# Performance work log

Measured on AMD Instinct MI355X. Metric: run time of the kernel, lower is better.

The kernel has to match this reference:

```python
import jax, jax.numpy as jnp
import numpy as np

BINS = 32


def _mi_from_hist(hist):
    # hist: (B, BINS, BINS) raw counts. Normalize and compute MI per sample,
    # matching np.histogram2d marginals (px from axis=1 sum, py from axis=0 sum).
    total = jnp.sum(hist, axis=(1, 2), keepdims=True)
    p = hist / total                      # joint pmf (B, BINS, BINS)
    px = jnp.sum(p, axis=2)               # (B, BINS)
    py = jnp.sum(p, axis=1)               # (B, BINS)
    denom = px[:, :, None] * py[:, None, :]
    pos = p > 0                           # p>0 implies px>0 and py>0
    ratio = jnp.where(pos, p / jnp.where(pos, denom, 1.0), 1.0)
    mi = jnp.sum(jnp.where(pos, p * jnp.log(ratio), 0.0), axis=(1, 2))
    return mi                             # (B,)


def setup_inputs() -> dict:
    key = jax.random.key(0)
    k1, k2 = jax.random.split(key)
    shape = (32, 2, 512, 512)
    return {
        "input": jax.random.normal(k1, shape, dtype=jnp.float32),
        "target": jax.random.normal(k2, shape, dtype=jnp.float32),
    }


def reference(input, target):
    B = input.shape[0]
    u = (input.reshape(B, -1) + 1.0) / 2.0   # (B, N) mapped to ~[0,1]
    v = (target.reshape(B, -1) + 1.0) / 2.0
    # np.histogram2d with range [[0,1],[0,1]] drops out-of-range points and
    # includes the right edge in the last bin.
    in_range = (u >= 0) & (u <= 1) & (v >= 0) & (v <= 1)
    w = in_range.astype(u.dtype)
    iu = jnp.clip(jnp.floor(u * BINS).astype(jnp.int32), 0, BINS - 1)
    iv = jnp.clip(jnp.floor(v * BINS).astype(jnp.int32), 0, BINS - 1)
    flat = (jnp.arange(B, dtype=jnp.int32)[:, None] * (BINS * BINS)
            + iu * BINS + iv).reshape(-1)
    hist = jax.ops.segment_sum(w.reshape(-1), flat,
                               num_segments=B * BINS * BINS)
    hist = hist.reshape(B, BINS, BINS)
    mi = _mi_from_hist(hist)
    return -jnp.mean(mi)
```

## Files before the change

### kernel.cpp

```cpp
#include <hip/hip_runtime.h>


#define BINS 32
#define NBINS2 1024
#define LDS_ROW 33
#define LDS_HIST (BINS * LDS_ROW)
#define NBATCH 32
#define N_PER_BATCH (2 * 512 * 512)
#define NVEC_BATCH (N_PER_BATCH / 4)
#define BPB 64
#define THREADS 256
#define VPT 8

__global__ __launch_bounds__(THREADS) void hist_kernel(const float* __restrict__ x,
                                                       const float* __restrict__ y,
                                                       unsigned* __restrict__ parts) {
    __shared__ unsigned h[LDS_HIST];
    for (int i = threadIdx.x; i < LDS_HIST; i += THREADS) h[i] = 0u;
    __syncthreads();

    const int b   = blockIdx.x >> 6;
    const int blk = blockIdx.x & 63;
    const float4* xb = (const float4*)x + (size_t)b * NVEC_BATCH;
    const float4* yb = (const float4*)y + (size_t)b * NVEC_BATCH;

    const int off = blk * THREADS + threadIdx.x;
    float4 xa[VPT], ya[VPT];
#pragma unroll
    for (int j = 0; j < VPT; ++j) xa[j] = xb[(size_t)j * (BPB * THREADS) + off];
#pragma unroll
    for (int j = 0; j < VPT; ++j) ya[j] = yb[(size_t)j * (BPB * THREADS) + off];

#pragma unroll
    for (int j = 0; j < VPT; ++j) {
        float ax[4] = {xa[j].x, xa[j].y, xa[j].z, xa[j].w};
        float ty[4] = {ya[j].x, ya[j].y, ya[j].z, ya[j].w};
#pragma unroll
        for (int k = 0; k < 4; ++k) {
            float u = (ax[k] + 1.0f) * 0.5f;
            float v = (ty[k] + 1.0f) * 0.5f;
            bool ok = (u >= 0.0f) & (u <= 1.0f) & (v >= 0.0f) & (v <= 1.0f);
            if (ok) {
                int iu = (int)(u * 32.0f); if (iu > 31) iu = 31;
                int iv = (int)(v * 32.0f); if (iv > 31) iv = 31;
                atomicAdd(&h[iu * LDS_ROW + iv], 1u);
            }
        }
    }
    __syncthreads();

    unsigned* g = parts + (size_t)blockIdx.x * NBINS2;
    for (int i = threadIdx.x; i < NBINS2; i += THREADS)
        g[i] = h[(i >> 5) * LDS_ROW + (i & 31)];
}

__global__ __launch_bounds__(1024) void mi_kernel(const unsigned* __restrict__ parts,
                                                  int nparts,
                                                  double* __restrict__ mi_out) {
    __shared__ unsigned c[NBINS2];
    __shared__ unsigned px[BINS];
    __shared__ unsigned py[BINS];
    __shared__ double red[16];

    const int b = blockIdx.x;
    const unsigned* base = parts + (size_t)b * nparts * NBINS2 + threadIdx.x;
    unsigned s = 0;
#pragma unroll 8
    for (int p = 0; p < nparts; ++p) s += base[(size_t)p * NBINS2];
    c[threadIdx.x] = s;
    __syncthreads();

    if (threadIdx.x < 32) {
        unsigned r = 0;
        for (int j = 0; j < 32; ++j) r += c[threadIdx.x * BINS + j];
        px[threadIdx.x] = r;
    } else if (threadIdx.x < 64) {
        int col = threadIdx.x - 32;
        unsigned r = 0;
        for (int j = 0; j < 32; ++j) r += c[j * BINS + col];
        py[col] = r;
    }
    __syncthreads();

    unsigned total = 0;
    for (int j = 0; j < 32; ++j) total += px[j];
    const double T = (double)total;

    double acc = 0.0;
    {
        unsigned cc = c[threadIdx.x];
        if (cc) {
            int r = threadIdx.x >> 5, col = threadIdx.x & 31;
            acc = (double)cc * log((double)cc * T / ((double)px[r] * (double)py[col]));
        }
    }
    for (int off = 32; off > 0; off >>= 1)
        acc += __shfl_down(acc, off, 64);
    int wave = threadIdx.x >> 6;
    if ((threadIdx.x & 63) == 0) red[wave] = acc;
    __syncthreads();
    if (threadIdx.x == 0) {
        double t = 0.0;
        for (int i = 0; i < 16; ++i) t += red[i];
        mi_out[b] = t / T;
    }
}

__global__ void finalize_kernel(const double* __restrict__ mi, float* __restrict__ out) {
    if (threadIdx.x == 0) {
        double s = 0.0;
        for (int i = 0; i < NBATCH; ++i) s += mi[i];
        out[0] = (float)(-s / (double)NBATCH);
    }
}

extern "C" void kernel_launch(void* const* d_in, const int* in_sizes, int n_in,
                              void* d_out, int out_size, void* d_ws, size_t ws_size,
                              hipStream_t stream) {
    const float* x = (const float*)d_in[0];
    const float* y = (const float*)d_in[1];
    float* out = (float*)d_out;

    unsigned* parts = (unsigned*)d_ws;
    double* mi = (double*)((char*)d_ws + (size_t)NBATCH * BPB * NBINS2 * sizeof(unsigned));

    hist_kernel<<<NBATCH * BPB, THREADS, 0, stream>>>(x, y, parts);
    mi_kernel<<<NBATCH, 1024, 0, stream>>>(parts, BPB, mi);
    finalize_kernel<<<1, 64, 0, stream>>>(mi, out);
}
```

Measured before the change: 35.65 us.

## Use fewer histogram blocks per batch with double-buffered register tile loads

Reduces histogram blocks per batch from 64 to 16, each processing four tiles of loads with a two-buffer register pipeline so the next tile's global loads are issued while the current one is binned into LDS. Fewer partial histograms cut the writeback traffic and the reduction work in mi_kernel, whose loop becomes fully unrolled over a compile-time count. The trade-off is fewer resident blocks for latency hiding and higher register use from the two buffers.

```diff
diff --git a/kernel.cpp b/kernel.cpp
--- a/kernel.cpp
+++ b/kernel.cpp
@@ -8,9 +8,10 @@
 #define NBATCH 32
 #define N_PER_BATCH (2 * 512 * 512)
 #define NVEC_BATCH (N_PER_BATCH / 4)
-#define BPB 64
+#define BPB 16
 #define THREADS 256
-#define VPT 8
+#define NTILE 4
+#define TV 8
 
 __global__ __launch_bounds__(THREADS) void hist_kernel(const float* __restrict__ x,
                                                        const float* __restrict__ y,
@@ -19,34 +20,51 @@
     for (int i = threadIdx.x; i < LDS_HIST; i += THREADS) h[i] = 0u;
     __syncthreads();
 
-    const int b   = blockIdx.x >> 6;
-    const int blk = blockIdx.x & 63;
+    const int b   = blockIdx.x / BPB;
+    const int blk = blockIdx.x % BPB;
     const float4* xb = (const float4*)x + (size_t)b * NVEC_BATCH;
     const float4* yb = (const float4*)y + (size_t)b * NVEC_BATCH;
+    const int off = blk * THREADS + threadIdx.x;
+    const int STRIDE = BPB * THREADS;
 
-    const int off = blk * THREADS + threadIdx.x;
-    float4 xa[VPT], ya[VPT];
-#pragma unroll
-    for (int j = 0; j < VPT; ++j) xa[j] = xb[(size_t)j * (BPB * THREADS) + off];
-#pragma unroll
-    for (int j = 0; j < VPT; ++j) ya[j] = yb[(size_t)j * (BPB * THREADS) + off];
+#define LOAD_TILE(XA, YA, T)                                                  \
+    _Pragma("unroll")                                                         \
+    for (int j = 0; j < TV; ++j)                                              \
+        XA[j] = xb[(size_t)((T) * TV + j) * STRIDE + off];                    \
+    _Pragma("unroll")                                                         \
+    for (int j = 0; j < TV; ++j)                                              \
+        YA[j] = yb[(size_t)((T) * TV + j) * STRIDE + off];
 
-#pragma unroll
-    for (int j = 0; j < VPT; ++j) {
-        float ax[4] = {xa[j].x, xa[j].y, xa[j].z, xa[j].w};
-        float ty[4] = {ya[j].x, ya[j].y, ya[j].z, ya[j].w};
-#pragma unroll
-        for (int k = 0; k < 4; ++k) {
-            float u = (ax[k] + 1.0f) * 0.5f;
-            float v = (ty[k] + 1.0f) * 0.5f;
-            bool ok = (u >= 0.0f) & (u <= 1.0f) & (v >= 0.0f) & (v <= 1.0f);
-            if (ok) {
-                int iu = (int)(u * 32.0f); if (iu > 31) iu = 31;
-                int iv = (int)(v * 32.0f); if (iv > 31) iv = 31;
-                atomicAdd(&h[iu * LDS_ROW + iv], 1u);
-            }
-        }
+#define CONSUME_TILE(XA, YA)                                                  \
+    _Pragma("unroll")                                                         \
+    for (int j = 0; j < TV; ++j) {                                            \
+        float ax[4] = {XA[j].x, XA[j].y, XA[j].z, XA[j].w};                   \
+        float ty[4] = {YA[j].x, YA[j].y, YA[j].z, YA[j].w};                   \
+        _Pragma("unroll")                                                     \
+        for (int k = 0; k < 4; ++k) {                                         \
+            float u = (ax[k] + 1.0f) * 0.5f;                                  \
+            float v = (ty[k] + 1.0f) * 0.5f;                                  \
+            bool ok = (u >= 0.0f) & (u <= 1.0f) & (v >= 0.0f) & (v <= 1.0f);  \
+            if (ok) {                                                         \
+                int iu = (int)(u * 32.0f); if (iu > 31) iu = 31;              \
+                int iv = (int)(v * 32.0f); if (iv > 31) iv = 31;              \
+                atomicAdd(&h[iu * LDS_ROW + iv], 1u);                         \
+            }                                                                 \
+        }                                                                     \
     }
+
+    float4 xA[TV], yA[TV], xB[TV], yB[TV];
+    LOAD_TILE(xA, yA, 0)
+    LOAD_TILE(xB, yB, 1)
+    CONSUME_TILE(xA, yA)
+    LOAD_TILE(xA, yA, 2)
+    CONSUME_TILE(xB, yB)
+    LOAD_TILE(xB, yB, 3)
+    CONSUME_TILE(xA, yA)
+    CONSUME_TILE(xB, yB)
+#undef LOAD_TILE
+#undef CONSUME_TILE
+
     __syncthreads();
 
     unsigned* g = parts + (size_t)blockIdx.x * NBINS2;
@@ -55,7 +73,6 @@
 }
 
 __global__ __launch_bounds__(1024) void mi_kernel(const unsigned* __restrict__ parts,
-                                                  int nparts,
                                                   double* __restrict__ mi_out) {
     __shared__ unsigned c[NBINS2];
     __shared__ unsigned px[BINS];
@@ -63,10 +80,10 @@
     __shared__ double red[16];
 
     const int b = blockIdx.x;
-    const unsigned* base = parts + (size_t)b * nparts * NBINS2 + threadIdx.x;
+    const unsigned* base = parts + (size_t)b * BPB * NBINS2 + threadIdx.x;
     unsigned s = 0;
-#pragma unroll 8
-    for (int p = 0; p < nparts; ++p) s += base[(size_t)p * NBINS2];
+#pragma unroll
+    for (int p = 0; p < BPB; ++p) s += base[(size_t)p * NBINS2];
     c[threadIdx.x] = s;
     __syncthreads();
 
@@ -125,6 +142,6 @@
     double* mi = (double*)((char*)d_ws + (size_t)NBATCH * BPB * NBINS2 * sizeof(unsigned));
 
     hist_kernel<<<NBATCH * BPB, THREADS, 0, stream>>>(x, y, parts);
-    mi_kernel<<<NBATCH, 1024, 0, stream>>>(parts, BPB, mi);
+    mi_kernel<<<NBATCH, 1024, 0, stream>>>(parts, mi);
     finalize_kernel<<<1, 64, 0, stream>>>(mi, out);
 }
```

After: 37.21 us. 1.04x slower.
